# Optimization experiments

Measured on AMD Instinct MI355X. Metric: run time of the kernel, lower is better.

## Reference

```python
import jax, jax.numpy as jnp
import numpy as np


def setup_inputs() -> dict:
    key = jax.random.key(0)
    ks = jax.random.split(key, 10)
    B, S, V, E, C = 256, 512, 50000, 300, 10
    sentences = jax.random.randint(ks[0], (B, S), 0, V)
    emb_table = jax.random.normal(ks[1], (V, E), dtype=jnp.float32) * 0.1
    # pad_token=0 row zeroed like nn.Embedding(padding_idx=0)
    emb_table = emb_table.at[0].set(0.0)
    k3 = jax.random.normal(ks[2], (3, E), dtype=jnp.float32) * 0.05
    b3 = jax.random.normal(ks[3], (1,), dtype=jnp.float32) * 0.05
    k4 = jax.random.normal(ks[4], (4, E), dtype=jnp.float32) * 0.05
    b4 = jax.random.normal(ks[5], (1,), dtype=jnp.float32) * 0.05
    k5 = jax.random.normal(ks[6], (5, E), dtype=jnp.float32) * 0.05
    b5 = jax.random.normal(ks[7], (1,), dtype=jnp.float32) * 0.05
    fc_w = jax.random.normal(ks[8], (C, 3), dtype=jnp.float32) * 0.1
    fc_b = jax.random.normal(ks[9], (C,), dtype=jnp.float32) * 0.1
    return {"sentences": sentences, "emb_table": emb_table,
            "k3": k3, "b3": b3, "k4": k4, "b4": b4, "k5": k5, "b5": b5,
            "fc_w": fc_w, "fc_b": fc_b}


def _window_feature(emb, k, b):
    # emb: [B,S,E]; k: [w,E]; conv with 1 in/1 out channel spanning full E (VALID)
    out = jax.lax.conv_general_dilated(
        emb[:, None, :, :],            # [B,1,S,E]
        k[None, None, :, :],           # [1,1,w,E]
        window_strides=(1, 1), padding="VALID")  # [B,1,S-w+1,1]
    f = jnp.tanh(out[:, 0, :, 0] + b)  # [B,S-w+1]
    return f.max(axis=-1)              # [B]


def reference(sentences, emb_table, k3, b3, k4, b4, k5, b5, fc_w, fc_b):
    emb = emb_table[sentences]  # [B,S,E]
    feats = jnp.stack([_window_feature(emb, k3, b3),
                       _window_feature(emb, k4, b4),
                       _window_feature(emb, k5, b5)], axis=-1)  # [B,3]
    # dropout is identity in eval mode
    logits = feats @ fc_w.T + fc_b  # [B,C]
    return jax.nn.log_softmax(logits, axis=-1)
```

## Files before the change

### kernel.cpp

```cpp
#include <hip/hip_runtime.h>
#include <hip/hip_bf16.h>
#include <math.h>

#define NSENT 256
#define SLEN  512
#define VROWS 50000
#define EDIM  300
#define NROW  12
#define SSTR  16
#define NSTEP 10

typedef __attribute__((ext_vector_type(8))) short bf16x8;
typedef __attribute__((ext_vector_type(4))) float f32x4;

static __device__ __forceinline__ short f2bf(float f) {
    __hip_bfloat16 h = __float2bfloat16(f);
    short s;
    __builtin_memcpy(&s, &h, sizeof(s));
    return s;
}

__global__ __launch_bounds__(256, 4)
void vocab_scores_mfma(const float* __restrict__ emb,
                       const float* __restrict__ k3,
                       const float* __restrict__ k4,
                       const float* __restrict__ k5,
                       float* __restrict__ s)
{
    __shared__ bf16x8 bfrag_lds[NSTEP * 64];

    const int tid  = threadIdx.x;
    const int lane = tid & 63;
    const int wave = tid >> 6;
    const int rc   = lane & 15;
    const int kg   = lane >> 4;

    for (int e = tid; e < NSTEP * 64; e += 256) {
        const int st  = e >> 6;
        const int le  = e & 63;
        const int rce = le & 15;
        const int kge = le >> 4;
        const float* krow = nullptr;
        if      (rce < 3)  krow = k3 + rce * EDIM;
        else if (rce < 7)  krow = k4 + (rce - 3) * EDIM;
        else if (rce < 12) krow = k5 + (rce - 7) * EDIM;
        const int k0 = st * 32 + kge * 8;
        float4 b0 = make_float4(0.f,0.f,0.f,0.f);
        float4 b1 = make_float4(0.f,0.f,0.f,0.f);
        if (krow) {
            if (k0 + 4 <= EDIM) b0 = *reinterpret_cast<const float4*>(krow + k0);
            if (k0 + 8 <= EDIM) b1 = *reinterpret_cast<const float4*>(krow + k0 + 4);
        }
        bf16x8 f;
        f[0]=f2bf(b0.x); f[1]=f2bf(b0.y); f[2]=f2bf(b0.z); f[3]=f2bf(b0.w);
        f[4]=f2bf(b1.x); f[5]=f2bf(b1.y); f[6]=f2bf(b1.z); f[7]=f2bf(b1.w);
        bfrag_lds[e] = f;
    }
    __syncthreads();

    const int vbase = blockIdx.x * 64 + wave * 16;
    const int vrow  = min(vbase + rc, VROWS - 1);
    const float* arow = emb + (size_t)vrow * EDIM;

    f32x4 acc = {0.f, 0.f, 0.f, 0.f};

    #pragma unroll
    for (int half = 0; half < 2; ++half) {
        float4 a0[5], a1[5];
        #pragma unroll
        for (int i = 0; i < 5; ++i) {
            const int k0 = (half * 5 + i) * 32 + kg * 8;
            a0[i] = (k0 + 4 <= EDIM)
                  ? *reinterpret_cast<const float4*>(arow + k0)
                  : make_float4(0.f,0.f,0.f,0.f);
            a1[i] = (k0 + 8 <= EDIM)
                  ? *reinterpret_cast<const float4*>(arow + k0 + 4)
                  : make_float4(0.f,0.f,0.f,0.f);
        }
        #pragma unroll
        for (int i = 0; i < 5; ++i) {
            const int st = half * 5 + i;
            const bf16x8 bf = bfrag_lds[st * 64 + lane];
            bf16x8 af;
            af[0]=f2bf(a0[i].x); af[1]=f2bf(a0[i].y);
            af[2]=f2bf(a0[i].z); af[3]=f2bf(a0[i].w);
            af[4]=f2bf(a1[i].x); af[5]=f2bf(a1[i].y);
            af[6]=f2bf(a1[i].z); af[7]=f2bf(a1[i].w);
            acc = __builtin_amdgcn_mfma_f32_16x16x32_bf16(af, bf, acc, 0, 0, 0);
        }
    }

    if (rc < NROW) {
        #pragma unroll
        for (int j = 0; j < 4; ++j) {
            const int v = vbase + kg * 4 + j;
            if (v < VROWS) s[(size_t)v * SSTR + rc] = acc[j];
        }
    }
}

__global__ __launch_bounds__(512, 1)
void textcnn_finish(const int*   __restrict__ sent,
                    const float* __restrict__ s,
                    const float* __restrict__ b3,
                    const float* __restrict__ b4,
                    const float* __restrict__ b5,
                    const float* __restrict__ fcw,
                    const float* __restrict__ fcb,
                    float* __restrict__ out)
{
    __shared__ float s_lds[NROW * SLEN];
    __shared__ float red[8][3];

    const int b = blockIdx.x;
    const int t = threadIdx.x;

    const int widx = sent[b * SLEN + t];
    const float4* row = reinterpret_cast<const float4*>(s + (size_t)widx * SSTR);
    const float4 sa = row[0];
    const float4 sb = row[1];
    const float4 sc = row[2];

    const float bb3 = b3[0], bb4 = b4[0], bb5 = b5[0];

    s_lds[ 0*SLEN + t] = sa.x;  s_lds[ 1*SLEN + t] = sa.y;
    s_lds[ 2*SLEN + t] = sa.z;  s_lds[ 3*SLEN + t] = sa.w;
    s_lds[ 4*SLEN + t] = sb.x;  s_lds[ 5*SLEN + t] = sb.y;
    s_lds[ 6*SLEN + t] = sb.z;  s_lds[ 7*SLEN + t] = sb.w;
    s_lds[ 8*SLEN + t] = sc.x;  s_lds[ 9*SLEN + t] = sc.y;
    s_lds[10*SLEN + t] = sc.z;  s_lds[11*SLEN + t] = sc.w;
    __syncthreads();

    float m3 = -1e30f, m4 = -1e30f, m5 = -1e30f;
    if (t < SLEN - 2)
        m3 = tanhf(s_lds[0*SLEN + t] + s_lds[1*SLEN + t+1] +
                   s_lds[2*SLEN + t+2] + bb3);
    if (t < SLEN - 3)
        m4 = tanhf(s_lds[3*SLEN + t] + s_lds[4*SLEN + t+1] +
                   s_lds[5*SLEN + t+2] + s_lds[6*SLEN + t+3] + bb4);
    if (t < SLEN - 4)
        m5 = tanhf(s_lds[7*SLEN + t] + s_lds[8*SLEN + t+1] +
                   s_lds[9*SLEN + t+2] + s_lds[10*SLEN + t+3] +
                   s_lds[11*SLEN + t+4] + bb5);

    #pragma unroll
    for (int off = 32; off; off >>= 1) {
        m3 = fmaxf(m3, __shfl_xor(m3, off));
        m4 = fmaxf(m4, __shfl_xor(m4, off));
        m5 = fmaxf(m5, __shfl_xor(m5, off));
    }
    if ((t & 63) == 0) {
        const int w = t >> 6;
        red[w][0] = m3; red[w][1] = m4; red[w][2] = m5;
    }
    __syncthreads();

    if (t == 0) {
        float f3 = red[0][0], f4 = red[0][1], f5 = red[0][2];
        #pragma unroll
        for (int w = 1; w < 8; ++w) {
            f3 = fmaxf(f3, red[w][0]);
            f4 = fmaxf(f4, red[w][1]);
            f5 = fmaxf(f5, red[w][2]);
        }
        float lg[10];
        float mx = -1e30f;
        #pragma unroll
        for (int c = 0; c < 10; ++c) {
            lg[c] = fcb[c] + f3 * fcw[c*3+0] + f4 * fcw[c*3+1] + f5 * fcw[c*3+2];
            mx = fmaxf(mx, lg[c]);
        }
        float ssum = 0.f;
        #pragma unroll
        for (int c = 0; c < 10; ++c) ssum += expf(lg[c] - mx);
        const float lse = logf(ssum);
        #pragma unroll
        for (int c = 0; c < 10; ++c) out[b * 10 + c] = lg[c] - mx - lse;
    }
}

extern "C" void kernel_launch(void* const* d_in, const int* in_sizes, int n_in,
                              void* d_out, int out_size, void* d_ws, size_t ws_size,
                              hipStream_t stream) {
    const int*   sent = (const int*)  d_in[0];
    const float* emb  = (const float*)d_in[1];
    const float* k3   = (const float*)d_in[2];
    const float* b3   = (const float*)d_in[3];
    const float* k4   = (const float*)d_in[4];
    const float* b4   = (const float*)d_in[5];
    const float* k5   = (const float*)d_in[6];
    const float* b5   = (const float*)d_in[7];
    const float* fcw  = (const float*)d_in[8];
    const float* fcb  = (const float*)d_in[9];
    float* out = (float*)d_out;
    float* s   = (float*)d_ws;

    const int nblk = (VROWS + 63) / 64;
    vocab_scores_mfma<<<nblk, 256, 0, stream>>>(emb, k3, k4, k5, s);
    textcnn_finish<<<NSENT, 512, 0, stream>>>(sent, s, b3, b4, b5, fcw, fcb, out);
}
```

Measured before the change: 23.86 us.

## Split each sentence across two blocks with atomic max merge and last-block epilogue

The finish kernel now launches two 256-thread blocks per sentence instead of one 512-thread block. Each block computes window maxima over half the positions, using a 4-position halo, and merges its result into global per-sentence features with an order-preserving unsigned atomicMax. A done counter lets the second block to finish compute the FC layer and log-softmax. This raises block count and occupancy for the small second kernel, at the cost of global atomics, fences, and initialising the features and counters in the first kernel.

Result: slower. 50.72 us (+112.5%).

```diff
diff --git a/kernel.cpp b/kernel.cpp
--- a/kernel.cpp
+++ b/kernel.cpp
@@ -9,6 +9,8 @@
 #define NROW  12
 #define SSTR  16
 #define NSTEP 10
+#define FEAT_OFF (4u << 20)
+#define DONE_OFF ((4u << 20) + 4096)
 
 typedef __attribute__((ext_vector_type(8))) short bf16x8;
 typedef __attribute__((ext_vector_type(4))) float f32x4;
@@ -20,12 +22,22 @@
     return s;
 }
 
+static __device__ __forceinline__ unsigned encf(float f) {
+    unsigned b = __float_as_uint(f);
+    return (b & 0x80000000u) ? ~b : (b | 0x80000000u);
+}
+static __device__ __forceinline__ float decf(unsigned u) {
+    return __uint_as_float((u & 0x80000000u) ? (u & 0x7FFFFFFFu) : ~u);
+}
+
 __global__ __launch_bounds__(256, 4)
 void vocab_scores_mfma(const float* __restrict__ emb,
                        const float* __restrict__ k3,
                        const float* __restrict__ k4,
                        const float* __restrict__ k5,
-                       float* __restrict__ s)
+                       float* __restrict__ s,
+                       unsigned* __restrict__ feats_u,
+                       unsigned* __restrict__ done)
 {
     __shared__ bf16x8 bfrag_lds[NSTEP * 64];
 
@@ -34,6 +46,14 @@
     const int wave = tid >> 6;
     const int rc   = lane & 15;
     const int kg   = lane >> 4;
+
+    if (blockIdx.x == 0 && tid < NSENT) {
+        const unsigned e = encf(-2.0f);
+        feats_u[tid * 3 + 0] = e;
+        feats_u[tid * 3 + 1] = e;
+        feats_u[tid * 3 + 2] = e;
+        done[tid] = 0u;
+    }
 
     for (int e = tid; e < NSTEP * 64; e += 256) {
         const int st  = e >> 6;
@@ -99,7 +119,7 @@
     }
 }
 
-__global__ __launch_bounds__(512, 1)
+__global__ __launch_bounds__(256, 4)
 void textcnn_finish(const int*   __restrict__ sent,
                     const float* __restrict__ s,
                     const float* __restrict__ b3,
@@ -107,41 +127,56 @@
                     const float* __restrict__ b5,
                     const float* __restrict__ fcw,
                     const float* __restrict__ fcb,
+                    unsigned* __restrict__ feats_u,
+                    unsigned* __restrict__ done,
                     float* __restrict__ out)
 {
-    __shared__ float s_lds[NROW * SLEN];
-    __shared__ float red[8][3];
-
-    const int b = blockIdx.x;
-    const int t = threadIdx.x;
-
-    const int widx = sent[b * SLEN + t];
+    __shared__ float P[NROW][260];
+    __shared__ float red[4][3];
+
+    const int blk  = blockIdx.x;
+    const int bs   = blk >> 1;
+    const int half = blk & 1;
+    const int t0   = half << 8;
+    const int tid  = threadIdx.x;
+    const int lane = tid & 63;
+    const int wave = tid >> 6;
+
+    const int widx = sent[bs * SLEN + t0 + tid];
     const float4* row = reinterpret_cast<const float4*>(s + (size_t)widx * SSTR);
     const float4 sa = row[0];
     const float4 sb = row[1];
     const float4 sc = row[2];
 
+    float4 ha, hb, hc;
+    const bool do_halo = (half == 0) && (tid < 4);
+    if (do_halo) {
+        const int wi2 = sent[bs * SLEN + 256 + tid];
+        const float4* r2 = reinterpret_cast<const float4*>(s + (size_t)wi2 * SSTR);
+        ha = r2[0]; hb = r2[1]; hc = r2[2];
+    }
     const float bb3 = b3[0], bb4 = b4[0], bb5 = b5[0];
 
-    s_lds[ 0*SLEN + t] = sa.x;  s_lds[ 1*SLEN + t] = sa.y;
-    s_lds[ 2*SLEN + t] = sa.z;  s_lds[ 3*SLEN + t] = sa.w;
-    s_lds[ 4*SLEN + t] = sb.x;  s_lds[ 5*SLEN + t] = sb.y;
-    s_lds[ 6*SLEN + t] = sb.z;  s_lds[ 7*SLEN + t] = sb.w;
-    s_lds[ 8*SLEN + t] = sc.x;  s_lds[ 9*SLEN + t] = sc.y;
-    s_lds[10*SLEN + t] = sc.z;  s_lds[11*SLEN + t] = sc.w;
+    P[ 0][tid]=sa.x; P[ 1][tid]=sa.y; P[ 2][tid]=sa.z; P[ 3][tid]=sa.w;
+    P[ 4][tid]=sb.x; P[ 5][tid]=sb.y; P[ 6][tid]=sb.z; P[ 7][tid]=sb.w;
+    P[ 8][tid]=sc.x; P[ 9][tid]=sc.y; P[10][tid]=sc.z; P[11][tid]=sc.w;
+    if (do_halo) {
+        const int h = 256 + tid;
+        P[ 0][h]=ha.x; P[ 1][h]=ha.y; P[ 2][h]=ha.z; P[ 3][h]=ha.w;
+        P[ 4][h]=hb.x; P[ 5][h]=hb.y; P[ 6][h]=hb.z; P[ 7][h]=hb.w;
+        P[ 8][h]=hc.x; P[ 9][h]=hc.y; P[10][h]=hc.z; P[11][h]=hc.w;
+    }
     __syncthreads();
 
-    float m3 = -1e30f, m4 = -1e30f, m5 = -1e30f;
-    if (t < SLEN - 2)
-        m3 = tanhf(s_lds[0*SLEN + t] + s_lds[1*SLEN + t+1] +
-                   s_lds[2*SLEN + t+2] + bb3);
-    if (t < SLEN - 3)
-        m4 = tanhf(s_lds[3*SLEN + t] + s_lds[4*SLEN + t+1] +
-                   s_lds[5*SLEN + t+2] + s_lds[6*SLEN + t+3] + bb4);
-    if (t < SLEN - 4)
-        m5 = tanhf(s_lds[7*SLEN + t] + s_lds[8*SLEN + t+1] +
-                   s_lds[9*SLEN + t+2] + s_lds[10*SLEN + t+3] +
-                   s_lds[11*SLEN + t+4] + bb5);
+    const int ts = t0 + tid;
+    float m3 = -2.0f, m4 = -2.0f, m5 = -2.0f;
+    if (ts < SLEN - 2)
+        m3 = tanhf(P[0][tid] + P[1][tid+1] + P[2][tid+2] + bb3);
+    if (ts < SLEN - 3)
+        m4 = tanhf(P[3][tid] + P[4][tid+1] + P[5][tid+2] + P[6][tid+3] + bb4);
+    if (ts < SLEN - 4)
+        m5 = tanhf(P[7][tid] + P[8][tid+1] + P[9][tid+2] + P[10][tid+3] +
+                   P[11][tid+4] + bb5);
 
     #pragma unroll
     for (int off = 32; off; off >>= 1) {
@@ -149,33 +184,46 @@
         m4 = fmaxf(m4, __shfl_xor(m4, off));
         m5 = fmaxf(m5, __shfl_xor(m5, off));
     }
-    if ((t & 63) == 0) {
-        const int w = t >> 6;
-        red[w][0] = m3; red[w][1] = m4; red[w][2] = m5;
-    }
+    if (lane == 0) { red[wave][0]=m3; red[wave][1]=m4; red[wave][2]=m5; }
     __syncthreads();
 
-    if (t == 0) {
+    if (tid == 0) {
         float f3 = red[0][0], f4 = red[0][1], f5 = red[0][2];
         #pragma unroll
-        for (int w = 1; w < 8; ++w) {
+        for (int w = 1; w < 4; ++w) {
             f3 = fmaxf(f3, red[w][0]);
             f4 = fmaxf(f4, red[w][1]);
             f5 = fmaxf(f5, red[w][2]);
         }
-        float lg[10];
-        float mx = -1e30f;
-        #pragma unroll
-        for (int c = 0; c < 10; ++c) {
-            lg[c] = fcb[c] + f3 * fcw[c*3+0] + f4 * fcw[c*3+1] + f5 * fcw[c*3+2];
-            mx = fmaxf(mx, lg[c]);
-        }
-        float ssum = 0.f;
-        #pragma unroll
-        for (int c = 0; c < 10; ++c) ssum += expf(lg[c] - mx);
-        const float lse = logf(ssum);
-        #pragma unroll
-        for (int c = 0; c < 10; ++c) out[b * 10 + c] = lg[c] - mx - lse;
+        atomicMax(&feats_u[bs * 3 + 0], encf(f3));
+        atomicMax(&feats_u[bs * 3 + 1], encf(f4));
+        atomicMax(&feats_u[bs * 3 + 2], encf(f5));
+        __threadfence();
+        const unsigned old = __hip_atomic_fetch_add(&done[bs], 1u,
+                                 __ATOMIC_ACQ_REL, __HIP_MEMORY_SCOPE_AGENT);
+        if (old == 1u) {
+            __threadfence();
+            const float g3 = decf(__hip_atomic_load(&feats_u[bs*3+0],
+                                  __ATOMIC_ACQUIRE, __HIP_MEMORY_SCOPE_AGENT));
+            const float g4 = decf(__hip_atomic_load(&feats_u[bs*3+1],
+                                  __ATOMIC_ACQUIRE, __HIP_MEMORY_SCOPE_AGENT));
+            const float g5 = decf(__hip_atomic_load(&feats_u[bs*3+2],
+                                  __ATOMIC_ACQUIRE, __HIP_MEMORY_SCOPE_AGENT));
+            float lg[10];
+            float mx = -1e30f;
+            #pragma unroll
+            for (int c = 0; c < 10; ++c) {
+                lg[c] = fcb[c] + g3 * fcw[c*3+0] + g4 * fcw[c*3+1]
+                               + g5 * fcw[c*3+2];
+                mx = fmaxf(mx, lg[c]);
+            }
+            float ssum = 0.f;
+            #pragma unroll
+            for (int c = 0; c < 10; ++c) ssum += expf(lg[c] - mx);
+            const float lse = logf(ssum);
+            #pragma unroll
+            for (int c = 0; c < 10; ++c) out[bs * 10 + c] = lg[c] - mx - lse;
+        }
     }
 }
 
@@ -194,8 +242,12 @@
     const float* fcb  = (const float*)d_in[9];
     float* out = (float*)d_out;
     float* s   = (float*)d_ws;
+    unsigned* feats_u = (unsigned*)((char*)d_ws + FEAT_OFF);
+    unsigned* done    = (unsigned*)((char*)d_ws + DONE_OFF);
 
     const int nblk = (VROWS + 63) / 64;
-    vocab_scores_mfma<<<nblk, 256, 0, stream>>>(emb, k3, k4, k5, s);
-    textcnn_finish<<<NSENT, 512, 0, stream>>>(sent, s, b3, b4, b5, fcw, fcb, out);
-}
+    vocab_scores_mfma<<<nblk, 256, 0, stream>>>(emb, k3, k4, k5, s,
+                                                feats_u, done);
+    textcnn_finish<<<NSENT * 2, 256, 0, stream>>>(sent, s, b3, b4, b5,
+                                                  fcw, fcb, feats_u, done, out);
+}
```

## Stage embedding tiles via direct global-to-LDS loads and split K across waves

Applied to the files above, without the earlier changes.

The vocab-scoring kernel now copies a contiguous 32-row embedding tile into LDS using global_load_lds async DMA, in fully coalesced 1KB chunks, instead of each lane doing strided per-row float4 loads. Each block handles 32 rows with the K dimension split between wave pairs, and partial MFMA accumulators are reduced through LDS. The aim is better coalescing and more bytes in flight on the bandwidth-bound scan of the 60MB table. In exchange it uses about 39KB of LDS per block, lowers the occupancy hint, doubles the block count, and adds an extra barrier and reduction step.

New measurement: 27.44 us. 15.0% more time.

```diff
diff --git a/kernel.cpp b/kernel.cpp
--- a/kernel.cpp
+++ b/kernel.cpp
@@ -9,6 +9,10 @@
 #define NROW  12
 #define SSTR  16
 #define NSTEP 10
+#define RPB   32
+#define TILEB (RPB * EDIM * 4)
+#define NCHUNK 38
+#define NBLKA ((VROWS + RPB - 1) / RPB)
 
 typedef __attribute__((ext_vector_type(8))) short bf16x8;
 typedef __attribute__((ext_vector_type(4))) float f32x4;
@@ -20,20 +24,37 @@
     return s;
 }
 
-__global__ __launch_bounds__(256, 4)
+__global__ __launch_bounds__(256, 3)
 void vocab_scores_mfma(const float* __restrict__ emb,
                        const float* __restrict__ k3,
                        const float* __restrict__ k4,
                        const float* __restrict__ k5,
                        float* __restrict__ s)
 {
+    __shared__ float4 ebuf4[NCHUNK * 64];
     __shared__ bf16x8 bfrag_lds[NSTEP * 64];
+    __shared__ f32x4  part[4][64];
 
     const int tid  = threadIdx.x;
     const int lane = tid & 63;
     const int wave = tid >> 6;
     const int rc   = lane & 15;
     const int kg   = lane >> 4;
+
+    char* ebuf = reinterpret_cast<char*>(ebuf4);
+    const size_t EMB_END = (size_t)VROWS * EDIM * 4;
+    const size_t tbase   = (size_t)blockIdx.x * TILEB;
+
+    for (int c = wave; c < NCHUNK; c += 4) {
+        size_t gb = tbase + (size_t)c * 1024 + (size_t)lane * 16;
+        if (gb > EMB_END - 16) gb = EMB_END - 16;
+        const void* gp = (const char*)emb + gb;
+        void* lp = ebuf + c * 1024;
+        __builtin_amdgcn_global_load_lds(
+            (const __attribute__((address_space(1))) void*)gp,
+            (__attribute__((address_space(3))) void*)lp,
+            16, 0, 0);
+    }
 
     for (int e = tid; e < NSTEP * 64; e += 256) {
         const int st  = e >> 6;
@@ -58,43 +79,36 @@
     }
     __syncthreads();
 
-    const int vbase = blockIdx.x * 64 + wave * 16;
-    const int vrow  = min(vbase + rc, VROWS - 1);
-    const float* arow = emb + (size_t)vrow * EDIM;
+    const int t = wave >> 1;
+    const int h = wave & 1;
+    const int lrow = t * 16 + rc;
 
     f32x4 acc = {0.f, 0.f, 0.f, 0.f};
-
     #pragma unroll
-    for (int half = 0; half < 2; ++half) {
-        float4 a0[5], a1[5];
-        #pragma unroll
-        for (int i = 0; i < 5; ++i) {
-            const int k0 = (half * 5 + i) * 32 + kg * 8;
-            a0[i] = (k0 + 4 <= EDIM)
-                  ? *reinterpret_cast<const float4*>(arow + k0)
-                  : make_float4(0.f,0.f,0.f,0.f);
-            a1[i] = (k0 + 8 <= EDIM)
-                  ? *reinterpret_cast<const float4*>(arow + k0 + 4)
-                  : make_float4(0.f,0.f,0.f,0.f);
-        }
-        #pragma unroll
-        for (int i = 0; i < 5; ++i) {
-            const int st = half * 5 + i;
-            const bf16x8 bf = bfrag_lds[st * 64 + lane];
-            bf16x8 af;
-            af[0]=f2bf(a0[i].x); af[1]=f2bf(a0[i].y);
-            af[2]=f2bf(a0[i].z); af[3]=f2bf(a0[i].w);
-            af[4]=f2bf(a1[i].x); af[5]=f2bf(a1[i].y);
-            af[6]=f2bf(a1[i].z); af[7]=f2bf(a1[i].w);
-            acc = __builtin_amdgcn_mfma_f32_16x16x32_bf16(af, bf, acc, 0, 0, 0);
-        }
-    }
-
-    if (rc < NROW) {
-        #pragma unroll
-        for (int j = 0; j < 4; ++j) {
-            const int v = vbase + kg * 4 + j;
-            if (v < VROWS) s[(size_t)v * SSTR + rc] = acc[j];
+    for (int st = 0; st < 5; ++st) {
+        const int koff = ((h * 5 + st) * 32 + kg * 8) * 4;
+        const char* p = ebuf + lrow * 1200 + koff;
+        const float4 f0 = *reinterpret_cast<const float4*>(p);
+        const float4 f1 = *reinterpret_cast<const float4*>(p + 16);
+        bf16x8 af;
+        af[0]=f2bf(f0.x); af[1]=f2bf(f0.y); af[2]=f2bf(f0.z); af[3]=f2bf(f0.w);
+        af[4]=f2bf(f1.x); af[5]=f2bf(f1.y); af[6]=f2bf(f1.z); af[7]=f2bf(f1.w);
+        const bf16x8 bf = bfrag_lds[(h * 5 + st) * 64 + lane];
+        acc = __builtin_amdgcn_mfma_f32_16x16x32_bf16(af, bf, acc, 0, 0, 0);
+    }
+
+    part[wave][lane] = acc;
+    __syncthreads();
+
+    if (wave < 2) {
+        const f32x4 p0 = part[wave * 2 + 0][lane];
+        const f32x4 p1 = part[wave * 2 + 1][lane];
+        if (rc < NROW) {
+            #pragma unroll
+            for (int j = 0; j < 4; ++j) {
+                const int v = blockIdx.x * RPB + wave * 16 + kg * 4 + j;
+                if (v < VROWS) s[(size_t)v * SSTR + rc] = p0[j] + p1[j];
+            }
         }
     }
 }
@@ -195,7 +209,6 @@
     float* out = (float*)d_out;
     float* s   = (float*)d_ws;
 
-    const int nblk = (VROWS + 63) / 64;
-    vocab_scores_mfma<<<nblk, 256, 0, stream>>>(emb, k3, k4, k5, s);
+    vocab_scores_mfma<<<NBLKA, 256, 0, stream>>>(emb, k3, k4, k5, s);
     textcnn_finish<<<NSENT, 512, 0, stream>>>(sent, s, b3, b4, b5, fcw, fcb, out);
 }
```
